# Optimization experiments

Hardware: AMD Instinct MI355X
Metric: run time of the kernel (lower is better)

## Reference

```python
import jax, jax.numpy as jnp
import numpy as np

B, T, DI, H, L = 32, 512, 512, 512, 4  # num_layers=4 -> 1 base LSTM + 3 CALSTM layers


def setup_inputs() -> dict:
    key = jax.random.key(0)
    ks = jax.random.split(key, 4)
    s_ih = 1.0 / np.sqrt(DI)
    s_hh = 1.0 / np.sqrt(H)
    s_ca = 1.0 / np.sqrt(2 * H)
    return {
        "x": jax.random.normal(ks[0], (B, T, DI), dtype=jnp.float32),
        "w_ih": jax.random.normal(ks[1], (4 * H, DI), dtype=jnp.float32) * s_ih,
        "w_hh": jax.random.normal(ks[2], (4 * H, H), dtype=jnp.float32) * s_hh,
        "b_ih": jnp.zeros((4 * H,), jnp.float32),
        "b_hh": jnp.zeros((4 * H,), jnp.float32),
        "ca_w": jax.random.normal(ks[3], (L - 1, 5 * H, 2 * H), dtype=jnp.float32) * s_ca,
        "ca_b": jnp.zeros((L - 1, 5 * H), jnp.float32),
    }


def _stacked_lstm(x, w_ih, w_hh, b_ih, b_hh, ca_w, ca_b):
    b = x.shape[0]
    z = jnp.zeros((b, H), x.dtype)
    bias = b_ih + b_hh

    # --- layer 0: StatefulLSTM (plain LSTM cell) ---
    def base_step(carry, x_t):
        h, c = carry
        m = x_t @ w_ih.T + h @ w_hh.T + bias  # (B, 4H)
        i, f, g, o = jnp.split(m, 4, axis=1)
        c = jax.nn.sigmoid(i) * jnp.tanh(g) + jax.nn.sigmoid(f) * c
        h = jax.nn.sigmoid(o) * jnp.tanh(c)
        return (h, c), (h, c)

    _, (hs, cs) = jax.lax.scan(base_step, (z, z), jnp.swapaxes(x, 0, 1))  # (T,B,H) each

    # --- layers 1..L-1: CALSTM with fuse_type='add' ---
    for l in range(ca_w.shape[0]):
        Wl, bl = ca_w[l], ca_b[l]

        def ca_step(carry, xt, Wl=Wl, bl=bl):
            h_prev, c_prev = carry
            h_low, c_low = xt
            m = jnp.concatenate([h_low, h_prev], axis=1) @ Wl.T + bl  # (B, 5H)
            i, f_prev, f_low, u, o = jnp.split(m, 5, axis=1)
            c = (c_prev * jax.nn.sigmoid(f_prev + 1.0)
                 + c_low * jax.nn.sigmoid(f_low + 1.0)
                 + jnp.tanh(u) * jax.nn.sigmoid(i))
            h = jax.nn.sigmoid(o) * jnp.tanh(c)
            return (h, c), (h, c)

        _, (hs, cs) = jax.lax.scan(ca_step, (z, z), (hs, cs))

    hs = jnp.swapaxes(hs, 0, 1)  # (B, T, H)
    cs = jnp.swapaxes(cs, 0, 1)
    return hs, cs


def reference(x, w_ih, w_hh, b_ih, b_hh, ca_w, ca_b):
    hs, cs = _stacked_lstm(x, w_ih, w_hh, b_ih, b_hh, ca_w, ca_b)
    # ((hs, cs), hx) with hx = last step state (length=None path)
    return (hs, cs, hs[:, -1], cs[:, -1])
```

## Files before the change

### kernel.cpp

```cpp
#include <hip/hip_runtime.h>
#include <math.h>


#define TT 512
#define HH 512
#define ROWP 1032
#define W_OFF 0
#define A_OFF 82560
#define RED_OFF A_OFF
#define LDS_BYTES (A_OFF + 66048)

#define CWS_OFF 98304
#define FL_OFF  294912
#define WS_ZERO_WORDS (FL_OFF + 1024)

typedef _Float16 half8 __attribute__((ext_vector_type(8)));
typedef float f32x4 __attribute__((ext_vector_type(4)));

__global__ void zero_ws_k(unsigned* __restrict__ ws){
    int i = blockIdx.x*blockDim.x + threadIdx.x;
    for (; i < WS_ZERO_WORDS; i += gridDim.x*blockDim.x) ws[i] = 0u;
}

__device__ __forceinline__ float sigm(float v){ return 1.f/(1.f+__expf(-v)); }

__device__ __forceinline__ void poll_layer(const unsigned* fl, int L, unsigned need){
    const int i = threadIdx.x & 63;
    const unsigned* p = fl + (L*64 + i)*4;
    for (;;){
        const unsigned v = __hip_atomic_load(p, __ATOMIC_RELAXED, __HIP_MEMORY_SCOPE_AGENT);
        if (__all((int)(v >= need))) break;
        __builtin_amdgcn_s_sleep(2);
    }
}

template<int MT>
__device__ void run_loop(const float* __restrict__ x, const float* __restrict__ b_ih,
                         const float* __restrict__ b_hh, const float* __restrict__ ca_b,
                         float* __restrict__ out, float* __restrict__ ws_f,
                         char* lds, int layer, int ub)
{
    const int tid  = threadIdx.x;
    const int lane = tid & 63;
    const int wv   = tid >> 6;
    const int i16  = lane & 15, qq = lane >> 4;
    unsigned short* hws = (unsigned short*)ws_f;
    float*    cws = ws_f + CWS_OFF;
    unsigned* fl  = (unsigned*)ws_f + FL_OFF;
    float* red = (float*)(lds + RED_OFF);

    const int gu = tid & 7, gb = tid >> 3, gj = ub*8 + gu;
    float bias[5] = {0,0,0,0,0};
    if (tid < 256){
        if (MT == 2){
#pragma unroll
            for (int g = 0; g < 4; ++g) bias[g] = b_ih[g*512+gj] + b_hh[g*512+gj];
        } else {
            const float* cbl = ca_b + (layer-1)*2560;
#pragma unroll
            for (int g = 0; g < 5; ++g) bias[g] = cbl[g*512+gj];
            bias[1] += 1.f; bias[2] += 1.f;
        }
    }
    if (tid == 0 && layer > 0)
        __hip_atomic_store(fl + (layer*64+ub)*4, (unsigned)layer,
                           __ATOMIC_RELAXED, __HIP_MEMORY_SCOPE_AGENT);

    float creg = 0.f;

    for (int tau = layer; tau < TT + layer; ++tau){
        const int t  = tau - layer;
        const int pb = tau % 3;
        const int qb = (tau + 2) % 3;

        uint4 xpk[8];
        if (MT == 2 && (tid & 127) < 64){
#pragma unroll
            for (int it = 0; it < 8; ++it){
                const int cidx = tid + it*512;
                const int b = cidx >> 7, kc = (cidx & 127) << 3;
                const float* xs = x + ((size_t)b*TT + t)*HH + kc;
                const float4 a = *(const float4*)xs;
                const float4 c = *(const float4*)(xs + 4);
                union { _Float16 h[8]; uint4 u; } pk;
                pk.h[0]=(_Float16)a.x; pk.h[1]=(_Float16)a.y;
                pk.h[2]=(_Float16)a.z; pk.h[3]=(_Float16)a.w;
                pk.h[4]=(_Float16)c.x; pk.h[5]=(_Float16)c.y;
                pk.h[6]=(_Float16)c.z; pk.h[7]=(_Float16)c.w;
                xpk[it] = pk.u;
            }
        }

        if (wv == 0)                    poll_layer(fl, layer,   (unsigned)tau);
        else if (wv == 1 && MT == 3)    poll_layer(fl, layer-1, (unsigned)tau);
        else if (wv == 2 && layer < 3)  poll_layer(fl, layer+1,
                                            (tau > 0) ? (unsigned)(tau-1) : 0u);
        if (wv == 0) __builtin_amdgcn_fence(__ATOMIC_ACQUIRE, "agent");
        __syncthreads();

        float clov = 0.f;
        if (MT == 3 && tid < 256)
            clov = cws[((layer-1)*3+qb)*16384 + gb*512 + gj];

        if (MT == 2){
            if ((tid & 127) < 64){
#pragma unroll
                for (int it = 0; it < 8; ++it){
                    const int cidx = tid + it*512;
                    const int b = cidx >> 7, kc = (cidx & 127) << 3;
                    *(uint4*)(lds + A_OFF + (size_t)(b*ROWP + kc)*2) = xpk[it];
                }
            } else {
                const unsigned short* hprev = hws + (layer*3+qb)*16384;
#pragma unroll
                for (int it = 0; it < 8; ++it){
                    const int cidx = tid + it*512;
                    const int b = cidx >> 7, kc = (cidx & 127) << 3;
                    const uint4 v = *(const uint4*)(hprev + b*512 + (kc - 512));
                    *(uint4*)(lds + A_OFF + (size_t)(b*ROWP + kc)*2) = v;
                }
            }
        } else {
            const unsigned short* hlow  = hws + ((layer-1)*3+qb)*16384;
            const unsigned short* hprev = hws + (layer*3+qb)*16384;
#pragma unroll
            for (int it = 0; it < 8; ++it){
                const int cidx = tid + it*512;
                const int b = cidx >> 7, kc = (cidx & 127) << 3;
                const uint4 v = (kc < 512) ? *(const uint4*)(hlow  + b*512 + kc)
                                           : *(const uint4*)(hprev + b*512 + (kc - 512));
                *(uint4*)(lds + A_OFF + (size_t)(b*ROWP + kc)*2) = v;
            }
        }
        __syncthreads();

        f32x4 acc[MT][2];
#pragma unroll
        for (int mt = 0; mt < MT; ++mt){ acc[mt][0] = (f32x4){0,0,0,0}; acc[mt][1] = (f32x4){0,0,0,0}; }
#pragma unroll
        for (int s = 0; s < 4; ++s){
            const int koff = wv*128 + s*32 + qq*8;
            half8 bfrag0 = *(const half8*)(lds + A_OFF + ((0*16 + i16)*ROWP + koff)*2);
            half8 bfrag1 = *(const half8*)(lds + A_OFF + ((1*16 + i16)*ROWP + koff)*2);
#pragma unroll
            for (int mt = 0; mt < MT; ++mt){
                half8 afrag = *(const half8*)(lds + W_OFF + ((mt*16 + i16)*ROWP + koff)*2);
                acc[mt][0] = __builtin_amdgcn_mfma_f32_16x16x32_f16(afrag, bfrag0, acc[mt][0], 0, 0, 0);
                acc[mt][1] = __builtin_amdgcn_mfma_f32_16x16x32_f16(afrag, bfrag1, acc[mt][1], 0, 0, 0);
            }
        }
        __syncthreads();

#pragma unroll
        for (int mt = 0; mt < MT; ++mt)
#pragma unroll
            for (int nt = 0; nt < 2; ++nt)
#pragma unroll
                for (int r = 0; r < 4; ++r)
                    red[((((wv*MT + mt)*2 + nt)*4 + r)*4 + qq)*16 + ((i16 + 4*r)&15)] = acc[mt][nt][r];
        __syncthreads();

        float hval = 0.f, cval = 0.f;
        if (tid < 256){
            const int NG = (MT == 2) ? 4 : 5;
            float mg[5];
#pragma unroll
            for (int g = 0; g < NG; ++g){
                const int m = g*8 + gu, mt2 = m >> 4, mr = m & 15, q2 = mr >> 2, r2 = mr & 3;
                const int nt2 = gb >> 4, i2 = gb & 15;
                const int base = (((mt2*2 + nt2)*4 + r2)*4 + q2)*16 + ((i2 + 4*r2)&15);
                float sm = 0.f;
#pragma unroll
                for (int kv = 0; kv < 8; ++kv) sm += red[base + kv*MT*512];
                mg[g] = sm + bias[g];
            }
            if (MT == 2){
                cval = sigm(mg[0])*tanhf(mg[2]) + sigm(mg[1])*creg;
                hval = sigm(mg[3])*tanhf(cval);
            } else {
                cval = creg*sigm(mg[1]) + clov*sigm(mg[2]) + tanhf(mg[3])*sigm(mg[0]);
                hval = sigm(mg[4])*tanhf(cval);
            }
            creg = cval;
        }

        const float hnb = __shfl_down(hval, 1);
        if (tid < 256){
            if (layer < 3)
                __hip_atomic_store(&cws[(layer*3+pb)*16384 + gb*512 + gj], cval,
                                   __ATOMIC_RELAXED, __HIP_MEMORY_SCOPE_AGENT);
            if ((gu & 1) == 0){
                union { _Float16 h2[2]; unsigned u; } pk;
                pk.h2[0] = (_Float16)hval; pk.h2[1] = (_Float16)hnb;
                __hip_atomic_store((unsigned*)(hws + (layer*3+pb)*16384 + gb*512 + gj),
                                   pk.u, __ATOMIC_RELAXED, __HIP_MEMORY_SCOPE_AGENT);
            }
        }
        asm volatile("s_waitcnt vmcnt(0)" ::: "memory");
        __syncthreads();
        if (tid == 0)
            __hip_atomic_store(fl + (layer*64+ub)*4, (unsigned)(tau + 1),
                               __ATOMIC_RELAXED, __HIP_MEMORY_SCOPE_AGENT);

        if (layer == 3 && tid < 256){
            const size_t pos = ((size_t)gb*TT + t)*HH + gj;
            out[pos]           = hval;
            out[8388608 + pos] = cval;
            if (t == TT-1){
                out[16777216 + (size_t)gb*HH + gj] = hval;
                out[16793600 + (size_t)gb*HH + gj] = cval;
            }
        }
    }
    if (tid == 0)
        __hip_atomic_store(fl + (layer*64+ub)*4, 0x7FFFFFFFu,
                           __ATOMIC_RELAXED, __HIP_MEMORY_SCOPE_AGENT);
}

__global__ __launch_bounds__(512) void persist_k(
    const float* __restrict__ x, const float* __restrict__ w_ih,
    const float* __restrict__ w_hh, const float* __restrict__ b_ih,
    const float* __restrict__ b_hh, const float* __restrict__ ca_w,
    const float* __restrict__ ca_b, float* __restrict__ out,
    float* __restrict__ ws_f)
{
    extern __shared__ char lds[];
    const int bx = blockIdx.x;
    const int layer = bx >> 6, ub = bx & 63;
    const int tid = threadIdx.x;
    const int rows = (layer == 0) ? 32 : 40;

    for (int idx = tid; idx < rows*256; idx += 512){
        const int r = idx >> 8, k4 = (idx & 255) * 4;
        const int g = r >> 3, u = r & 7;
        const int grow = g*512 + ub*8 + u;
        const float* src;
        if (layer == 0) src = (k4 < 512) ? (w_ih + (size_t)grow*512 + k4)
                                         : (w_hh + (size_t)grow*512 + (k4 - 512));
        else            src = ca_w + (size_t)(layer-1)*2560*1024 + (size_t)grow*1024 + k4;
        const float4 v = *(const float4*)src;
        union { _Float16 h[4]; uint2 u2; } pk;
        pk.h[0]=(_Float16)v.x; pk.h[1]=(_Float16)v.y;
        pk.h[2]=(_Float16)v.z; pk.h[3]=(_Float16)v.w;
        *(uint2*)(lds + W_OFF + ((size_t)(r*ROWP + k4))*2) = pk.u2;
    }
    if (layer == 0) run_loop<2>(x, b_ih, b_hh, ca_b, out, ws_f, lds, layer, ub);
    else            run_loop<3>(x, b_ih, b_hh, ca_b, out, ws_f, lds, layer, ub);
}

extern "C" void kernel_launch(void* const* d_in, const int* in_sizes, int n_in,
                              void* d_out, int out_size, void* d_ws, size_t ws_size,
                              hipStream_t stream)
{
    const float* x    = (const float*)d_in[0];
    const float* w_ih = (const float*)d_in[1];
    const float* w_hh = (const float*)d_in[2];
    const float* b_ih = (const float*)d_in[3];
    const float* b_hh = (const float*)d_in[4];
    const float* ca_w = (const float*)d_in[5];
    const float* ca_b = (const float*)d_in[6];
    float* out = (float*)d_out;
    float* ws  = (float*)d_ws;

    (void)hipFuncSetAttribute((const void*)persist_k,
                              hipFuncAttributeMaxDynamicSharedMemorySize, LDS_BYTES);
    hipLaunchKernelGGL(zero_ws_k, dim3(64), dim3(256), 0, stream, (unsigned*)ws);
    hipLaunchKernelGGL(persist_k, dim3(256), dim3(512), LDS_BYTES, stream,
                       x, w_ih, w_hh, b_ih, b_hh, ca_w, ca_b, out, ws);
}
```

Baseline: 3.157 ms.

## Replace flag polling with step-tagged h/c words for inter-block sync

Each h value is now stored as a 32-bit word with fp16 data in the low half and the timestep tag in the high half, and each c value as a (value, tag) pair. Consumers spin-load the data directly until the tags match, instead of waiting on per-block flags and then reading in a separate step. Flag polling stays only for buffer-reuse (WAR) safety, three steps back. This removes a round trip through flags and acquire fences on the critical recurrence path. The cost is double the workspace traffic for h, a static device global instead of the provided workspace, and bounded spin loops that could silently proceed if the cap is hit.

After: 3.944 ms. 24.9% more time.

```diff
diff --git a/kernel.cpp b/kernel.cpp
--- a/kernel.cpp
+++ b/kernel.cpp
@@ -10,24 +10,49 @@
 #define RED_OFF A_OFF
 #define LDS_BYTES (A_OFF + 66048)
 
-#define CWS_OFF 98304
-#define FL_OFF  294912
-#define WS_ZERO_WORDS (FL_OFF + 1024)
+#define CWS_OFF   196608
+#define FL_OFF    491520
+#define WS_ZERO_WORDS 492544
+
+#define SPIN_CAP (1u<<16)
 
 typedef _Float16 half8 __attribute__((ext_vector_type(8)));
 typedef float f32x4 __attribute__((ext_vector_type(4)));
-
-__global__ void zero_ws_k(unsigned* __restrict__ ws){
+typedef unsigned uint32x4 __attribute__((ext_vector_type(4)));
+typedef unsigned uint32x2 __attribute__((ext_vector_type(2)));
+
+__device__ __align__(16) unsigned g_ws[WS_ZERO_WORDS];
+
+__global__ void zero_ws_k(int dummy){
+    (void)dummy;
     int i = blockIdx.x*blockDim.x + threadIdx.x;
-    for (; i < WS_ZERO_WORDS; i += gridDim.x*blockDim.x) ws[i] = 0u;
+    for (; i < WS_ZERO_WORDS; i += gridDim.x*blockDim.x)
+        __hip_atomic_store(g_ws + i, 0u, __ATOMIC_RELAXED, __HIP_MEMORY_SCOPE_AGENT);
 }
 
 __device__ __forceinline__ float sigm(float v){ return 1.f/(1.f+__expf(-v)); }
+
+__device__ __forceinline__ void ld4_sys(uint32x4& d, const unsigned* p){
+    asm volatile("global_load_dwordx4 %0, %1, off sc0 sc1" : "=&v"(d) : "v"(p));
+}
+__device__ __forceinline__ void ld2_sys(uint32x2& d, const unsigned* p){
+    asm volatile("global_load_dwordx2 %0, %1, off sc0 sc1" : "=&v"(d) : "v"(p));
+}
+__device__ __forceinline__ void st1_sys(unsigned* p, unsigned v){
+    asm volatile("global_store_dword %0, %1, off sc0 sc1" :: "v"(p), "v"(v) : "memory");
+}
+__device__ __forceinline__ void st2_sys(unsigned* p, uint32x2 v){
+    asm volatile("global_store_dwordx2 %0, %1, off sc0 sc1" :: "v"(p), "v"(v) : "memory");
+}
+__device__ __forceinline__ void wait_vm0(){
+    asm volatile("s_waitcnt vmcnt(0)" ::: "memory");
+    __builtin_amdgcn_sched_barrier(0);
+}
 
 __device__ __forceinline__ void poll_layer(const unsigned* fl, int L, unsigned need){
     const int i = threadIdx.x & 63;
     const unsigned* p = fl + (L*64 + i)*4;
-    for (;;){
+    for (unsigned spin = 0; spin < SPIN_CAP; ++spin){
         const unsigned v = __hip_atomic_load(p, __ATOMIC_RELAXED, __HIP_MEMORY_SCOPE_AGENT);
         if (__all((int)(v >= need))) break;
         __builtin_amdgcn_s_sleep(2);
@@ -37,16 +62,15 @@
 template<int MT>
 __device__ void run_loop(const float* __restrict__ x, const float* __restrict__ b_ih,
                          const float* __restrict__ b_hh, const float* __restrict__ ca_b,
-                         float* __restrict__ out, float* __restrict__ ws_f,
-                         char* lds, int layer, int ub)
+                         float* __restrict__ out, char* lds, int layer, int ub)
 {
     const int tid  = threadIdx.x;
     const int lane = tid & 63;
     const int wv   = tid >> 6;
     const int i16  = lane & 15, qq = lane >> 4;
-    unsigned short* hws = (unsigned short*)ws_f;
-    float*    cws = ws_f + CWS_OFF;
-    unsigned* fl  = (unsigned*)ws_f + FL_OFF;
+    unsigned* hws = g_ws;
+    unsigned* cwsw = g_ws + CWS_OFF;
+    unsigned* fl  = g_ws + FL_OFF;
     float* red = (float*)(lds + RED_OFF);
 
     const int gu = tid & 7, gb = tid >> 3, gj = ub*8 + gu;
@@ -62,18 +86,52 @@
             bias[1] += 1.f; bias[2] += 1.f;
         }
     }
-    if (tid == 0 && layer > 0)
-        __hip_atomic_store(fl + (layer*64+ub)*4, (unsigned)layer,
-                           __ATOMIC_RELAXED, __HIP_MEMORY_SCOPE_AGENT);
 
     float creg = 0.f;
+
+    const bool hstage = (MT == 3) || ((tid & 127) >= 64);
 
     for (int tau = layer; tau < TT + layer; ++tau){
         const int t  = tau - layer;
         const int pb = tau % 3;
         const int qb = (tau + 2) % 3;
-
-        uint4 xpk[8];
+        const unsigned want = (unsigned)tau;
+
+        unsigned* hprev_u = hws + (layer*3 + qb)*16384;
+        unsigned* hlow_u  = (MT == 3) ? hws + ((layer-1)*3 + qb)*16384 : (unsigned*)0;
+
+        uint32x4 hv[16];
+        const unsigned* ap[8];
+        bool fab[8];
+        if (hstage){
+            const unsigned fw = want << 16;
+            const uint32x4 fresh0 = {fw, fw, fw, fw};
+#pragma unroll
+            for (int it = 0; it < 8; ++it){
+                const int cidx = tid + it*512;
+                const int b = cidx >> 7, kc = (cidx & 127) << 3;
+                const bool isprev = (MT == 2) || (kc >= 512);
+                const unsigned* src = (MT == 2)
+                    ? (hprev_u + b*512 + (kc - 512))
+                    : ((kc < 512) ? (hlow_u + b*512 + kc)
+                                  : (hprev_u + b*512 + (kc - 512)));
+                ap[it] = src;
+                fab[it] = (t == 0) && isprev;
+                if (fab[it]){
+                    hv[it*2] = fresh0; hv[it*2+1] = fresh0;
+                } else {
+                    ld4_sys(hv[it*2],   src);
+                    ld4_sys(hv[it*2+1], src + 4);
+                }
+            }
+        }
+        uint32x2 cl = {0u, 0u};
+        const unsigned* clp = (const unsigned*)0;
+        if (MT == 3 && tid < 256){
+            clp = cwsw + 2*(((layer-1)*3 + qb)*16384 + gb*512 + gj);
+            ld2_sys(cl, clp);
+        }
+        uint32x4 xpk[8];
         if (MT == 2 && (tid & 127) < 64){
 #pragma unroll
             for (int it = 0; it < 8; ++it){
@@ -82,7 +140,7 @@
                 const float* xs = x + ((size_t)b*TT + t)*HH + kc;
                 const float4 a = *(const float4*)xs;
                 const float4 c = *(const float4*)(xs + 4);
-                union { _Float16 h[8]; uint4 u; } pk;
+                union { _Float16 h[8]; uint32x4 u; } pk;
                 pk.h[0]=(_Float16)a.x; pk.h[1]=(_Float16)a.y;
                 pk.h[2]=(_Float16)a.z; pk.h[3]=(_Float16)a.w;
                 pk.h[4]=(_Float16)c.x; pk.h[5]=(_Float16)c.y;
@@ -91,46 +149,53 @@
             }
         }
 
-        if (wv == 0)                    poll_layer(fl, layer,   (unsigned)tau);
-        else if (wv == 1 && MT == 3)    poll_layer(fl, layer-1, (unsigned)tau);
-        else if (wv == 2 && layer < 3)  poll_layer(fl, layer+1,
-                                            (tau > 0) ? (unsigned)(tau-1) : 0u);
-        if (wv == 0) __builtin_amdgcn_fence(__ATOMIC_ACQUIRE, "agent");
-        __syncthreads();
-
-        float clov = 0.f;
-        if (MT == 3 && tid < 256)
-            clov = cws[((layer-1)*3+qb)*16384 + gb*512 + gj];
-
-        if (MT == 2){
-            if ((tid & 127) < 64){
+        if (hstage || (MT == 3 && tid < 256)) wait_vm0();
+
+        if (hstage){
+            for (unsigned spin = 0; spin < SPIN_CAP; ++spin){
+                bool any = false;
 #pragma unroll
                 for (int it = 0; it < 8; ++it){
-                    const int cidx = tid + it*512;
-                    const int b = cidx >> 7, kc = (cidx & 127) << 3;
-                    *(uint4*)(lds + A_OFF + (size_t)(b*ROWP + kc)*2) = xpk[it];
+                    if (fab[it]) continue;
+#pragma unroll
+                    for (int h2 = 0; h2 < 2; ++h2){
+                        uint32x4& v = hv[it*2 + h2];
+                        const bool st = ((v[0]>>16)!=want) || ((v[1]>>16)!=want) ||
+                                        ((v[2]>>16)!=want) || ((v[3]>>16)!=want);
+                        if (st){ any = true; ld4_sys(v, ap[it] + h2*4); }
+                    }
                 }
-            } else {
-                const unsigned short* hprev = hws + (layer*3+qb)*16384;
-#pragma unroll
-                for (int it = 0; it < 8; ++it){
-                    const int cidx = tid + it*512;
-                    const int b = cidx >> 7, kc = (cidx & 127) << 3;
-                    const uint4 v = *(const uint4*)(hprev + b*512 + (kc - 512));
-                    *(uint4*)(lds + A_OFF + (size_t)(b*ROWP + kc)*2) = v;
-                }
-            }
-        } else {
-            const unsigned short* hlow  = hws + ((layer-1)*3+qb)*16384;
-            const unsigned short* hprev = hws + (layer*3+qb)*16384;
+                if (__all((int)(!any))) break;
+                wait_vm0();
+            }
+        }
+
+        if (MT == 2 && (tid & 127) < 64){
 #pragma unroll
             for (int it = 0; it < 8; ++it){
                 const int cidx = tid + it*512;
                 const int b = cidx >> 7, kc = (cidx & 127) << 3;
-                const uint4 v = (kc < 512) ? *(const uint4*)(hlow  + b*512 + kc)
-                                           : *(const uint4*)(hprev + b*512 + (kc - 512));
-                *(uint4*)(lds + A_OFF + (size_t)(b*ROWP + kc)*2) = v;
-            }
+                *(uint32x4*)(lds + A_OFF + (size_t)(b*ROWP + kc)*2) = xpk[it];
+            }
+        }
+        if (hstage){
+#pragma unroll
+            for (int it = 0; it < 8; ++it){
+                const int cidx = tid + it*512;
+                const int b = cidx >> 7, kc = (cidx & 127) << 3;
+                const uint32x4 v0 = hv[it*2], v1 = hv[it*2+1];
+                uint32x4 p;
+                p[0] = (v0[0] & 0xffffu) | (v0[1] << 16);
+                p[1] = (v0[2] & 0xffffu) | (v0[3] << 16);
+                p[2] = (v1[0] & 0xffffu) | (v1[1] << 16);
+                p[3] = (v1[2] & 0xffffu) | (v1[3] << 16);
+                *(uint32x4*)(lds + A_OFF + (size_t)(b*ROWP + kc)*2) = p;
+            }
+        }
+
+        if (tau >= layer + 3){
+            if (wv == 2)                   poll_layer(fl, layer,   (unsigned)(tau-2));
+            else if (wv == 3 && layer < 3) poll_layer(fl, layer+1, (unsigned)(tau-2));
         }
         __syncthreads();
 
@@ -173,6 +238,14 @@
 #pragma unroll
                 for (int kv = 0; kv < 8; ++kv) sm += red[base + kv*MT*512];
                 mg[g] = sm + bias[g];
+            }
+            float clov = 0.f;
+            if (MT == 3){
+                for (unsigned spin = 0; cl[1] != want && spin < SPIN_CAP; ++spin){
+                    ld2_sys(cl, clp);
+                    wait_vm0();
+                }
+                clov = __uint_as_float(cl[0]);
             }
             if (MT == 2){
                 cval = sigm(mg[0])*tanhf(mg[2]) + sigm(mg[1])*creg;
@@ -182,24 +255,18 @@
                 hval = sigm(mg[4])*tanhf(cval);
             }
             creg = cval;
-        }
-
-        const float hnb = __shfl_down(hval, 1);
-        if (tid < 256){
-            if (layer < 3)
-                __hip_atomic_store(&cws[(layer*3+pb)*16384 + gb*512 + gj], cval,
-                                   __ATOMIC_RELAXED, __HIP_MEMORY_SCOPE_AGENT);
-            if ((gu & 1) == 0){
-                union { _Float16 h2[2]; unsigned u; } pk;
-                pk.h2[0] = (_Float16)hval; pk.h2[1] = (_Float16)hnb;
-                __hip_atomic_store((unsigned*)(hws + (layer*3+pb)*16384 + gb*512 + gj),
-                                   pk.u, __ATOMIC_RELAXED, __HIP_MEMORY_SCOPE_AGENT);
-            }
-        }
-        asm volatile("s_waitcnt vmcnt(0)" ::: "memory");
+
+            union { _Float16 f; unsigned short s; } cvt; cvt.f = (_Float16)hval;
+            const unsigned hw = (unsigned)cvt.s | ((unsigned)(tau + 1) << 16);
+            st1_sys(hws + ((layer*3 + pb)*16384 + gb*512 + gj), hw);
+            if (layer < 3){
+                uint32x2 cw = {__float_as_uint(cval), (unsigned)(tau + 1)};
+                st2_sys(cwsw + 2*((layer*3 + pb)*16384 + gb*512 + gj), cw);
+            }
+        }
         __syncthreads();
         if (tid == 0)
-            __hip_atomic_store(fl + (layer*64+ub)*4, (unsigned)(tau + 1),
+            __hip_atomic_store(fl + (layer*64 + ub)*4, (unsigned)tau,
                                __ATOMIC_RELAXED, __HIP_MEMORY_SCOPE_AGENT);
 
         if (layer == 3 && tid < 256){
@@ -212,17 +279,13 @@
             }
         }
     }
-    if (tid == 0)
-        __hip_atomic_store(fl + (layer*64+ub)*4, 0x7FFFFFFFu,
-                           __ATOMIC_RELAXED, __HIP_MEMORY_SCOPE_AGENT);
 }
 
 __global__ __launch_bounds__(512) void persist_k(
     const float* __restrict__ x, const float* __restrict__ w_ih,
     const float* __restrict__ w_hh, const float* __restrict__ b_ih,
     const float* __restrict__ b_hh, const float* __restrict__ ca_w,
-    const float* __restrict__ ca_b, float* __restrict__ out,
-    float* __restrict__ ws_f)
+    const float* __restrict__ ca_b, float* __restrict__ out)
 {
     extern __shared__ char lds[];
     const int bx = blockIdx.x;
@@ -239,13 +302,13 @@
                                          : (w_hh + (size_t)grow*512 + (k4 - 512));
         else            src = ca_w + (size_t)(layer-1)*2560*1024 + (size_t)grow*1024 + k4;
         const float4 v = *(const float4*)src;
-        union { _Float16 h[4]; uint2 u2; } pk;
+        union { _Float16 h[4]; uint32x2 u2; } pk;
         pk.h[0]=(_Float16)v.x; pk.h[1]=(_Float16)v.y;
         pk.h[2]=(_Float16)v.z; pk.h[3]=(_Float16)v.w;
-        *(uint2*)(lds + W_OFF + ((size_t)(r*ROWP + k4))*2) = pk.u2;
+        *(uint32x2*)(lds + W_OFF + ((size_t)(r*ROWP + k4))*2) = pk.u2;
     }
-    if (layer == 0) run_loop<2>(x, b_ih, b_hh, ca_b, out, ws_f, lds, layer, ub);
-    else            run_loop<3>(x, b_ih, b_hh, ca_b, out, ws_f, lds, layer, ub);
+    if (layer == 0) run_loop<2>(x, b_ih, b_hh, ca_b, out, lds, layer, ub);
+    else            run_loop<3>(x, b_ih, b_hh, ca_b, out, lds, layer, ub);
 }
 
 extern "C" void kernel_launch(void* const* d_in, const int* in_sizes, int n_in,
@@ -260,11 +323,11 @@
     const float* ca_w = (const float*)d_in[5];
     const float* ca_b = (const float*)d_in[6];
     float* out = (float*)d_out;
-    float* ws  = (float*)d_ws;
+    (void)d_ws; (void)ws_size;
 
     (void)hipFuncSetAttribute((const void*)persist_k,
                               hipFuncAttributeMaxDynamicSharedMemorySize, LDS_BYTES);
-    hipLaunchKernelGGL(zero_ws_k, dim3(64), dim3(256), 0, stream, (unsigned*)ws);
+    hipLaunchKernelGGL(zero_ws_k, dim3(64), dim3(256), 0, stream, 0);
     hipLaunchKernelGGL(persist_k, dim3(256), dim3(512), LDS_BYTES, stream,
-                       x, w_ih, w_hh, b_ih, b_hh, ca_w, ca_b, out, ws);
-}
+                       x, w_ih, w_hh, b_ih, b_hh, ca_w, ca_b, out);
+}
```
